# Optimization experiments

Hardware: AMD Instinct MI355X
Metric: run time of the kernel (lower is better)

The kernel has to match this reference:

```python
import jax, jax.numpy as jnp
import numpy as np

N, DIM, RF_DIM, H, W, PN, TOPK = 16, 2048, 256, 16, 8, 64, 10  # TOPK = 2*k = 2*(K//2)


def conv1x1(w, x):
    # w: [O, C] (1x1 conv kernel), x: [b, C, h, w] -> [b, O, h, w]
    return jnp.einsum('oc,bchw->bohw', w, x)


def calibration(x, y):
    # x, y: [b, c, h, w]
    b, c, h, w = x.shape
    xv = x.reshape(b, c, h * w)
    yv = y.reshape(b, c, h * w)
    c_aff = jax.nn.softmax(jnp.einsum('bcm,bdm->bcd', xv, yv), axis=2)  # [b,c,c]
    s_aff = jax.nn.softmax(jnp.einsum('bcm,bcn->bmn', xv, yv), axis=2)  # [b,hw,hw]
    c_avg = c_aff.mean(axis=-1)  # [b,c]
    s_avg = s_aff.mean(axis=-1)  # [b,hw]
    aff = (c_avg[:, :, None] * s_avg[:, None, :]).reshape(b, c, h, w)
    pos = jax.nn.relu(aff - 0.5) + 0.5
    comp = jax.nn.relu(0.5 - aff) + 0.5
    return x * pos + y * comp


def instance_norm(x, eps=1e-5):
    m = x.mean(axis=(2, 3), keepdims=True)
    v = x.var(axis=(2, 3), keepdims=True)
    return (x - m) * jax.lax.rsqrt(v + eps)


def setup_inputs():
    key = jax.random.key(0)
    ks = jax.random.split(key, 6)
    return {
        'inputs': jax.random.normal(ks[0], (N, DIM, H, W), jnp.float32),
        'mv_prototype': jax.random.normal(ks[1], (PN, DIM, H, W), jnp.float32),
        'w_rf': jax.random.normal(ks[2], (RF_DIM, DIM), jnp.float32) * 0.02,
        'w_rf_mv': jax.random.normal(ks[3], (DIM, TOPK * RF_DIM), jnp.float32) * 0.02,
        'w_rm_s': jax.random.normal(ks[4], (DIM, DIM), jnp.float32) * 0.02,
        'w_fuse': jax.random.normal(ks[5], (DIM, DIM), jnp.float32) * 0.02,
    }


def reference(inputs, mv_prototype, w_rf, w_rf_mv, w_rm_s, w_fuse):
    n, c, h, w = inputs.shape
    # pairwise squared euclidean distance (addmm-style cdist)
    xf = inputs.reshape(n, -1)
    pf = mv_prototype.reshape(mv_prototype.shape[0], -1)
    dist = (xf * xf).sum(1, keepdims=True) + (pf * pf).sum(1)[None, :] - 2.0 * xf @ pf.T
    idx = jnp.argsort(dist, axis=1)[:, :TOPK]  # [n, 2k] nearest prototypes
    # refine prototypes then gather per-sample top-2k and stack channels
    xp = conv1x1(w_rf, mv_prototype)  # [pn, rf_dim, h, w]
    mv_list = xp[idx].reshape(n, TOPK * RF_DIM, h, w)
    mvl = conv1x1(w_rf_mv, mv_list)  # [n, dim, h, w]
    mvl = jax.nn.relu(calibration(inputs, mvl))
    mv_a = instance_norm(conv1x1(w_rm_s, mvl))
    x_fuse = jax.nn.sigmoid(conv1x1(w_fuse, mv_a))
    return inputs + inputs * x_fuse
```

## Files before the change

kernel.cpp:

```cpp
#include <hip/hip_runtime.h>
#include <cstdint>
#include <cstddef>

#define N_    16
#define DIM_  2048
#define RF_   256
#define PN_   64
#define TOPK_ 10
#define HW_   128
#define KFULL (DIM_*HW_)
#define KMV   (TOPK_*RF_)

#define AS1 __attribute__((address_space(1)))
#define AS3 __attribute__((address_space(3)))

typedef __attribute__((ext_vector_type(8))) short bf16x8;
typedef __attribute__((ext_vector_type(4))) float f32x4;
typedef __attribute__((ext_vector_type(8))) unsigned short u16x8;

__device__ __forceinline__ unsigned short f2bf(float f) {
  unsigned u = __builtin_bit_cast(unsigned, f);
  unsigned r = (u + 0x7FFFu + ((u >> 16) & 1u)) >> 16;
  return (unsigned short)r;
}

__global__ __launch_bounds__(256)
void front_kernel(const float* __restrict__ x, const float* __restrict__ proto,
                  float* __restrict__ part,
                  unsigned short* __restrict__ protoT, float* __restrict__ pnorm_part,
                  const float* __restrict__ s0, const float* __restrict__ s1,
                  const float* __restrict__ s2, const float* __restrict__ s3,
                  unsigned short* __restrict__ d0, unsigned short* __restrict__ d1,
                  unsigned short* __restrict__ d2, unsigned short* __restrict__ d3,
                  float* __restrict__ dsum) {
  __shared__ alignas(16) unsigned char ldsbuf[43520];
  const int t = threadIdx.x;
  const int bid = blockIdx.x;
  {
    int g = bid * 256 + t;
    if (g < 1152) dsum[g] = 0.f;
  }

  if (bid < 512) {
    float (*xl)[16][68] = (float (*)[16][68])ldsbuf;
    float (*pl)[64][68] = (float (*)[64][68])(ldsbuf + 8704);
    const int b = bid;
    const int n0 = t & 7, pb = t >> 3;
    const int xr = t >> 4, xc = (t & 15) * 4;
    float acc[2][2] = {};
    const size_t kbase = (size_t)b * 512;

    float4 rx, rp[4];
    auto gload = [&](int ph) {
      const size_t k0 = kbase + ph * 64;
      rx = *(const float4*)(x + (size_t)xr * KFULL + k0 + xc);
#pragma unroll
      for (int i = 0; i < 4; ++i) {
        int idx = i * 256 + t;
        rp[i] = *(const float4*)(proto + (size_t)(idx >> 4) * KFULL + k0 + (idx & 15) * 4);
      }
    };
    auto swrite = [&](int buf) {
      *(float4*)&xl[buf][xr][xc] = rx;
#pragma unroll
      for (int i = 0; i < 4; ++i) {
        int idx = i * 256 + t;
        *(float4*)&pl[buf][idx >> 4][(idx & 15) * 4] = rp[i];
      }
    };

    gload(0); swrite(0);
    __syncthreads();
    for (int ph = 0; ph < 8; ++ph) {
      const int buf = ph & 1;
      if (ph + 1 < 8) gload(ph + 1);
#pragma unroll 8
      for (int k = 0; k < 64; k += 4) {
        float4 xa = *(float4*)&xl[buf][n0][k];
        float4 xb = *(float4*)&xl[buf][n0 + 8][k];
        float4 p0 = *(float4*)&pl[buf][pb][k];
        float4 p1 = *(float4*)&pl[buf][pb + 32][k];
        acc[0][0] += xa.x*p0.x + xa.y*p0.y + xa.z*p0.z + xa.w*p0.w;
        acc[0][1] += xa.x*p1.x + xa.y*p1.y + xa.z*p1.z + xa.w*p1.w;
        acc[1][0] += xb.x*p0.x + xb.y*p0.y + xb.z*p0.z + xb.w*p0.w;
        acc[1][1] += xb.x*p1.x + xb.y*p1.y + xb.z*p1.z + xb.w*p1.w;
      }
      if (ph + 1 < 8) swrite(buf ^ 1);
      __syncthreads();
    }

    float* scratch = (float*)ldsbuf;
    scratch[n0 * 64 + pb]            = -2.f * acc[0][0];
    scratch[n0 * 64 + pb + 32]       = -2.f * acc[0][1];
    scratch[(n0 + 8) * 64 + pb]      = -2.f * acc[1][0];
    scratch[(n0 + 8) * 64 + pb + 32] = -2.f * acc[1][1];
    __syncthreads();
    *(float4*)(part + (size_t)b * 1024 + t * 4) = *(const float4*)&scratch[t * 4];

  } else if (bid < 4608) {
    float (*tile)[129] = (float (*)[129])ldsbuf;
    float* ssq = (float*)(ldsbuf + 16512);
    const int local = bid - 512;
    const int p = local & 63;
    const int c0 = (local >> 6) * 32;
    const float* sp = proto + ((size_t)p * DIM_ + c0) * HW_;
    float sq = 0.f;
#pragma unroll
    for (int i = 0; i < 4; ++i) {
      int g = i * 256 + t;
      int ci = g >> 5, s4 = g & 31;
      float4 v = *(const float4*)(sp + (size_t)ci * HW_ + s4 * 4);
      sq += v.x * v.x + v.y * v.y + v.z * v.z + v.w * v.w;
      int sb = s4 * 4;
      tile[ci][sb] = v.x; tile[ci][sb + 1] = v.y; tile[ci][sb + 2] = v.z; tile[ci][sb + 3] = v.w;
    }
#pragma unroll
    for (int m = 1; m < 64; m <<= 1) sq += __shfl_xor(sq, m, 64);
    if ((t & 63) == 0) ssq[t >> 6] = sq;
    __syncthreads();
    if (t == 0) pnorm_part[(local >> 6) * PN_ + p] = ssq[0] + ssq[1] + ssq[2] + ssq[3];
    unsigned short* dp = protoT + (size_t)p * HW_ * DIM_ + (size_t)(c0 >> 3) * 1024;
#pragma unroll
    for (int i = 0; i < 2; ++i) {
      int cidx = i * 256 + t;
      int kg = cidx >> 7, s = cidx & 127;
      u16x8 pk;
#pragma unroll
      for (int u = 0; u < 8; ++u) pk[u] = f2bf(tile[kg * 8 + u][s]);
      *(u16x8*)(dp + (size_t)kg * 1024 + (size_t)s * 8) = pk;
    }

  } else {
    u16x8 (*ctile)[65] = (u16x8 (*)[65])ldsbuf;
    int local = bid - 4608;
    const float* s; unsigned short* d; int O, CG, tb;
    if (local < 32)       { s = s0; d = d0; O = RF_;  CG = DIM_ / 8; tb = local; }
    else if (local < 352) { s = s1; d = d1; O = DIM_; CG = KMV  / 8; tb = local - 32; }
    else if (local < 608) { s = s2; d = d2; O = DIM_; CG = DIM_ / 8; tb = local - 352; }
    else                  { s = s3; d = d3; O = DIM_; CG = DIM_ / 8; tb = local - 608; }
    const int nCgT = CG / 32;
    const int o0  = (tb / nCgT) * 64;
    const int cg0 = (tb % nCgT) * 32;
    const size_t C = (size_t)CG * 8;

#pragma unroll
    for (int i = 0; i < 8; ++i) {
      int idx = i * 256 + t, ol = idx >> 5, cg = idx & 31;
      const float* sp = s + (size_t)(o0 + ol) * C + (size_t)(cg0 + cg) * 8;
      float4 a = *(const float4*)sp;
      float4 b = *(const float4*)(sp + 4);
      u16x8 pk;
      pk[0] = f2bf(a.x); pk[1] = f2bf(a.y); pk[2] = f2bf(a.z); pk[3] = f2bf(a.w);
      pk[4] = f2bf(b.x); pk[5] = f2bf(b.y); pk[6] = f2bf(b.z); pk[7] = f2bf(b.w);
      ctile[cg][ol] = pk;
    }
    __syncthreads();
#pragma unroll
    for (int i = 0; i < 8; ++i) {
      int idx = i * 256 + t, cg = idx >> 6, ol = idx & 63;
      *(u16x8*)(d + (size_t)(cg0 + cg) * ((size_t)O * 8) + (size_t)(o0 + ol) * 8) =
          ctile[cg][ol];
    }
  }
}

__global__ __launch_bounds__(512)
void select_kernel(const float* __restrict__ part, const float* __restrict__ pnorm_part,
                   int* __restrict__ idx, int* __restrict__ flags) {
  __shared__ float red[8][64];
  __shared__ float sh[64];
  const int n = blockIdx.x, t = threadIdx.x;
  const int c = t & 63, ch = t >> 6;
  const float* pp = part + (size_t)ch * 64 * 1024 + n * 64 + c;
  float a0 = 0.f, a1 = 0.f, a2 = 0.f, a3 = 0.f;
  for (int b = 0; b < 64; b += 4) {
    a0 += pp[(size_t)(b + 0) * 1024];
    a1 += pp[(size_t)(b + 1) * 1024];
    a2 += pp[(size_t)(b + 2) * 1024];
    a3 += pp[(size_t)(b + 3) * 1024];
  }
  red[ch][c] = (a0 + a1) + (a2 + a3);
  __syncthreads();
  if (t < 64) {
    float pn = 0.f;
#pragma unroll 8
    for (int cb = 0; cb < DIM_ / 32; ++cb) pn += pnorm_part[cb * PN_ + t];
    float dv = pn;
#pragma unroll
    for (int i = 0; i < 8; ++i) dv += red[i][t];
    sh[t] = dv;
  }
  __syncthreads();
  if (t < 64) {
    float dval = sh[t];
    int rank = 0;
#pragma unroll
    for (int j = 0; j < 64; ++j) {
      float o = sh[j];
      rank += (o < dval || (o == dval && j < t)) ? 1 : 0;
    }
    if (rank < TOPK_) { idx[n * TOPK_ + rank] = t; flags[t] = 1; }
  }
}

#define BM 64
#define BKK 64

template <int MODE>
__global__ __launch_bounds__(512, 4)
void mfma_gemm_kernel(const unsigned short* __restrict__ Wb,
                      const unsigned short* __restrict__ Xb,
                      void* __restrict__ OutP,
                      const float* __restrict__ inputs,
                      const int* __restrict__ idxp,
                      const int* __restrict__ flags,
                      int K, int O, int Ldim) {
  __shared__ alignas(16) unsigned short Al[3][8 * BM * 8];
  __shared__ alignas(16) unsigned short Bl[3][8 * 128 * 8];

  const int t = threadIdx.x;
  const int w = t >> 6;
  const int lane = t & 63;
  const int q = lane >> 4;
  const int l15 = lane & 15;
  const int mq = w >> 1;
  const int h  = w & 1;
  const int batch = blockIdx.y;
  const int o0 = blockIdx.x * BM;

  if (MODE == 0 && flags && !flags[batch]) return;

  int idreg = 0;
  if (MODE == 1 && lane < TOPK_) idreg = idxp[batch * TOPK_ + lane];

  f32x4 acc[4] = {};

  auto issue = [&](int k0, int buf) {
    {
      const unsigned short* ga =
          Wb + (size_t)((k0 >> 3) + w) * (O * 8) + (size_t)(o0 + lane) * 8;
      __builtin_amdgcn_global_load_lds((const AS1 void*)ga,
                                       (AS3 void*)(&Al[buf][w * 512]), 16, 0, 0);
    }
    const unsigned short* base;
    if (MODE == 1) {
      int id = __shfl(idreg, k0 >> 8, 64);
      base = Xb + (size_t)id * (HW_ * RF_) + (size_t)((k0 & 255) >> 3) * 1024;
    } else {
      base = Xb + (size_t)batch * HW_ * K + (size_t)(k0 >> 3) * 1024;
    }
#pragma unroll
    for (int i = 0; i < 2; ++i) {
      int v = w * 2 + i;
      int qk = v >> 1, hh = v & 1;
      const unsigned short* gb = base + (size_t)qk * 1024 + (size_t)(hh * 64 + lane) * 8;
      __builtin_amdgcn_global_load_lds((const AS1 void*)gb,
                                       (AS3 void*)(&Bl[buf][qk * 1024 + hh * 512]), 16, 0, 0);
    }
  };

  const int nIter = K / BKK;

  issue(0, 0);
  issue(BKK, 1);

  for (int it = 0; it < nIter; ++it) {
    const int buf = it % 3;
    if (it + 1 < nIter) {
      asm volatile("s_waitcnt vmcnt(3)" ::: "memory");
    } else {
      asm volatile("s_waitcnt vmcnt(0)" ::: "memory");
    }
    __builtin_amdgcn_s_barrier();
#pragma unroll
    for (int s = 0; s < 2; ++s) {
      bf16x8 af, bfr[4];
      af = *(const bf16x8*)(&Al[buf][(s * 4 + q) * 512 + (mq * 16 + l15) * 8]);
#pragma unroll
      for (int nt = 0; nt < 4; ++nt)
        bfr[nt] = *(const bf16x8*)(&Bl[buf][(s * 4 + q) * 1024 + (h * 64 + nt * 16 + l15) * 8]);
#pragma unroll
      for (int nt = 0; nt < 4; ++nt)
        acc[nt] = __builtin_amdgcn_mfma_f32_16x16x32_bf16(af, bfr[nt], acc[nt], 0, 0, 0);
    }
    if (it + 2 < nIter) issue((it + 2) * BKK, (it + 2) % 3);
  }

  const float CAL = 1.0f - 1.0f / 262144.0f;

  float* nsumS = (float*)&Al[0][0];
  float* nsqS  = (float*)&Al[0][0] + 128;

  if (MODE == 2) {
#pragma unroll
    for (int reg = 0; reg < 4; ++reg) {
      float s_ = 0.f, q_ = 0.f;
#pragma unroll
      for (int nt = 0; nt < 4; ++nt) {
        float v = acc[nt][reg];
        s_ += v; q_ += v * v;
      }
#pragma unroll
      for (int m = 1; m < 16; m <<= 1) {
        s_ += __shfl_xor(s_, m, 64);
        q_ += __shfl_xor(q_, m, 64);
      }
      if (l15 == 0) {
        nsumS[w * 16 + q * 4 + reg] = s_;
        nsqS [w * 16 + q * 4 + reg] = q_;
      }
    }
    __syncthreads();
  }

  if (MODE == 3) {
    float* ofb = (float*)OutP + (size_t)batch * DIM_ * HW_;
    const float* inb = inputs + (size_t)batch * DIM_ * HW_;
#pragma unroll
    for (int nt = 0; nt < 4; ++nt) {
      int o = o0 + mq * 16 + q * 4;
      int s = h * 64 + nt * 16 + l15;
      f32x4 v = acc[nt];
#pragma unroll
      for (int g = 0; g < 4; ++g) {
        float in = inb[(size_t)(o + g) * HW_ + s];
        float sg = 1.f / (1.f + expf(-v[g]));
        ofb[(size_t)(o + g) * HW_ + s] = in * (1.f + sg);
      }
    }
  } else {
    unsigned short* ob = (unsigned short*)OutP + (size_t)batch * HW_ * Ldim;
    const float* inb = (MODE == 1) ? inputs + (size_t)batch * DIM_ * HW_ : nullptr;
    float mean[4], rs[4];
    if (MODE == 2) {
#pragma unroll
      for (int reg = 0; reg < 4; ++reg) {
        int ol = q * 4 + reg;
        float ts = nsumS[(mq * 2 + 0) * 16 + ol] + nsumS[(mq * 2 + 1) * 16 + ol];
        float tq = nsqS [(mq * 2 + 0) * 16 + ol] + nsqS [(mq * 2 + 1) * 16 + ol];
        float mn = ts * (1.f / 128.f);
        float vr = tq * (1.f / 128.f) - mn * mn;
        mean[reg] = mn; rs[reg] = rsqrtf(vr + 1e-5f);
      }
    }
#pragma unroll
    for (int nt = 0; nt < 4; ++nt) {
      int o = o0 + mq * 16 + q * 4;
      int s = h * 64 + nt * 16 + l15;
      f32x4 v = acc[nt];
      float r[4];
      if (MODE == 0) {
#pragma unroll
        for (int g = 0; g < 4; ++g) r[g] = v[g];
      } else if (MODE == 1) {
        const float* ip = inb + (size_t)o * HW_ + s;
#pragma unroll
        for (int g = 0; g < 4; ++g)
          r[g] = fmaxf(0.f, 0.5f * ip[(size_t)g * HW_] + CAL * v[g]);
      } else {
#pragma unroll
        for (int g = 0; g < 4; ++g) r[g] = (v[g] - mean[g]) * rs[g];
      }
      ushort4 pk;
      pk.x = f2bf(r[0]); pk.y = f2bf(r[1]); pk.z = f2bf(r[2]); pk.w = f2bf(r[3]);
      *(ushort4*)(ob + (size_t)(o >> 3) * 1024 + (size_t)s * 8 + (o & 7)) = pk;
    }
  }
}

extern "C" void kernel_launch(void* const* d_in, const int* in_sizes, int n_in,
                              void* d_out, int out_size, void* d_ws, size_t ws_size,
                              hipStream_t stream) {
  const float* inputs = (const float*)d_in[0];
  const float* proto  = (const float*)d_in[1];
  const float* w_rf   = (const float*)d_in[2];
  const float* w_rfmv = (const float*)d_in[3];
  const float* w_rms  = (const float*)d_in[4];
  const float* w_fuse = (const float*)d_in[5];
  float* out = (float*)d_out;

  uint8_t* ws = (uint8_t*)d_ws;
  size_t off = 0;
  auto alloc = [&](size_t bytes) { uint8_t* p = ws + off; off += (bytes + 255) & ~(size_t)255; return p; };

  float* dsum  = (float*)alloc(1088 * 4);
  int*   flags = (int*)alloc(PN_ * 4);
  int*   idx   = (int*)alloc(N_ * TOPK_ * 4);
  float* pnorm = (float*)alloc((size_t)(DIM_ / 32) * PN_ * 4);
  float* part  = (float*)alloc((size_t)512 * 1024 * 4);
  unsigned short* wrf_b   = (unsigned short*)alloc((size_t)RF_ * DIM_ * 2);
  unsigned short* wrfmv_b = (unsigned short*)alloc((size_t)DIM_ * KMV * 2);
  unsigned short* wrms_b  = (unsigned short*)alloc((size_t)DIM_ * DIM_ * 2);
  unsigned short* wfuse_b = (unsigned short*)alloc((size_t)DIM_ * DIM_ * 2);
  unsigned short* xpT     = (unsigned short*)alloc((size_t)PN_ * HW_ * RF_ * 2);
  unsigned short* protoT  = (unsigned short*)alloc((size_t)PN_ * HW_ * DIM_ * 2);
  unsigned short* mvlT = protoT;
  unsigned short* mvaT = protoT + (size_t)N_ * HW_ * DIM_;

  front_kernel<<<5472, 256, 0, stream>>>(inputs, proto, part, protoT, pnorm,
                                         w_rf, w_rfmv, w_rms, w_fuse,
                                         wrf_b, wrfmv_b, wrms_b, wfuse_b, dsum);
  select_kernel<<<N_, 512, 0, stream>>>(part, pnorm, idx, flags);

  mfma_gemm_kernel<0><<<dim3(RF_ / BM, PN_), 512, 0, stream>>>(
      wrf_b, protoT, xpT, nullptr, nullptr, flags, DIM_, RF_, RF_);
  mfma_gemm_kernel<1><<<dim3(DIM_ / BM, N_), 512, 0, stream>>>(
      wrfmv_b, xpT, mvlT, inputs, idx, nullptr, KMV, DIM_, DIM_);
  mfma_gemm_kernel<2><<<dim3(DIM_ / BM, N_), 512, 0, stream>>>(
      wrms_b, mvlT, mvaT, nullptr, nullptr, nullptr, DIM_, DIM_, DIM_);
  mfma_gemm_kernel<3><<<dim3(DIM_ / BM, N_), 512, 0, stream>>>(
      wfuse_b, mvaT, out, inputs, nullptr, nullptr, DIM_, DIM_, DIM_);
}
```

Before: 303.0 us.

## Fuse cdist dot-product into prototype transpose blocks, removing separate distance blocks

The 512 dedicated cross-product blocks are removed. Each prototype transpose block now keeps its loaded prototype slice in registers and dots it against all 16 inputs for the same channel range, writing a much smaller per-channel-block partial array. This lets the prototype be read once instead of twice and shrinks the partial buffer the select kernel reduces. In exchange, each transpose block rereads the input slices, 16 per block and 4096 blocks in total, relying on cache reuse, and does more register and shuffle work per block. Launch bounds with an occupancy hint and a smaller LDS buffer are also set.

```diff
diff --git a/kernel.cpp b/kernel.cpp
--- a/kernel.cpp
+++ b/kernel.cpp
@@ -24,16 +24,16 @@
   return (unsigned short)r;
 }
 
-__global__ __launch_bounds__(256)
+__global__ __launch_bounds__(256, 4)
 void front_kernel(const float* __restrict__ x, const float* __restrict__ proto,
-                  float* __restrict__ part,
                   unsigned short* __restrict__ protoT, float* __restrict__ pnorm_part,
+                  float* __restrict__ part2,
                   const float* __restrict__ s0, const float* __restrict__ s1,
                   const float* __restrict__ s2, const float* __restrict__ s3,
                   unsigned short* __restrict__ d0, unsigned short* __restrict__ d1,
                   unsigned short* __restrict__ d2, unsigned short* __restrict__ d3,
                   float* __restrict__ dsum) {
-  __shared__ alignas(16) unsigned char ldsbuf[43520];
+  __shared__ alignas(16) unsigned char ldsbuf[33280];
   const int t = threadIdx.x;
   const int bid = blockIdx.x;
   {
@@ -41,84 +41,48 @@
     if (g < 1152) dsum[g] = 0.f;
   }
 
-  if (bid < 512) {
-    float (*xl)[16][68] = (float (*)[16][68])ldsbuf;
-    float (*pl)[64][68] = (float (*)[64][68])(ldsbuf + 8704);
-    const int b = bid;
-    const int n0 = t & 7, pb = t >> 3;
-    const int xr = t >> 4, xc = (t & 15) * 4;
-    float acc[2][2] = {};
-    const size_t kbase = (size_t)b * 512;
-
-    float4 rx, rp[4];
-    auto gload = [&](int ph) {
-      const size_t k0 = kbase + ph * 64;
-      rx = *(const float4*)(x + (size_t)xr * KFULL + k0 + xc);
-#pragma unroll
-      for (int i = 0; i < 4; ++i) {
-        int idx = i * 256 + t;
-        rp[i] = *(const float4*)(proto + (size_t)(idx >> 4) * KFULL + k0 + (idx & 15) * 4);
-      }
-    };
-    auto swrite = [&](int buf) {
-      *(float4*)&xl[buf][xr][xc] = rx;
-#pragma unroll
-      for (int i = 0; i < 4; ++i) {
-        int idx = i * 256 + t;
-        *(float4*)&pl[buf][idx >> 4][(idx & 15) * 4] = rp[i];
-      }
-    };
-
-    gload(0); swrite(0);
-    __syncthreads();
-    for (int ph = 0; ph < 8; ++ph) {
-      const int buf = ph & 1;
-      if (ph + 1 < 8) gload(ph + 1);
-#pragma unroll 8
-      for (int k = 0; k < 64; k += 4) {
-        float4 xa = *(float4*)&xl[buf][n0][k];
-        float4 xb = *(float4*)&xl[buf][n0 + 8][k];
-        float4 p0 = *(float4*)&pl[buf][pb][k];
-        float4 p1 = *(float4*)&pl[buf][pb + 32][k];
-        acc[0][0] += xa.x*p0.x + xa.y*p0.y + xa.z*p0.z + xa.w*p0.w;
-        acc[0][1] += xa.x*p1.x + xa.y*p1.y + xa.z*p1.z + xa.w*p1.w;
-        acc[1][0] += xb.x*p0.x + xb.y*p0.y + xb.z*p0.z + xb.w*p0.w;
-        acc[1][1] += xb.x*p1.x + xb.y*p1.y + xb.z*p1.z + xb.w*p1.w;
-      }
-      if (ph + 1 < 8) swrite(buf ^ 1);
-      __syncthreads();
-    }
-
-    float* scratch = (float*)ldsbuf;
-    scratch[n0 * 64 + pb]            = -2.f * acc[0][0];
-    scratch[n0 * 64 + pb + 32]       = -2.f * acc[0][1];
-    scratch[(n0 + 8) * 64 + pb]      = -2.f * acc[1][0];
-    scratch[(n0 + 8) * 64 + pb + 32] = -2.f * acc[1][1];
-    __syncthreads();
-    *(float4*)(part + (size_t)b * 1024 + t * 4) = *(const float4*)&scratch[t * 4];
-
-  } else if (bid < 4608) {
+  if (bid < 4096) {
     float (*tile)[129] = (float (*)[129])ldsbuf;
     float* ssq = (float*)(ldsbuf + 16512);
-    const int local = bid - 512;
-    const int p = local & 63;
-    const int c0 = (local >> 6) * 32;
+    float (*dred)[16] = (float (*)[16])(ldsbuf + 16528);
+    const int p  = bid & 63;
+    const int cb = bid >> 6;
+    const int c0 = cb * 32;
     const float* sp = proto + ((size_t)p * DIM_ + c0) * HW_;
     float sq = 0.f;
+    float4 pv[4];
 #pragma unroll
     for (int i = 0; i < 4; ++i) {
       int g = i * 256 + t;
       int ci = g >> 5, s4 = g & 31;
       float4 v = *(const float4*)(sp + (size_t)ci * HW_ + s4 * 4);
+      pv[i] = v;
       sq += v.x * v.x + v.y * v.y + v.z * v.z + v.w * v.w;
       int sb = s4 * 4;
       tile[ci][sb] = v.x; tile[ci][sb + 1] = v.y; tile[ci][sb + 2] = v.z; tile[ci][sb + 3] = v.w;
     }
+
+    float accn[16];
+#pragma unroll
+    for (int n = 0; n < 16; ++n) accn[n] = 0.f;
+#pragma unroll
+    for (int n = 0; n < 16; ++n) {
+      const float* xb = x + (size_t)n * KFULL + (size_t)c0 * HW_;
+#pragma unroll
+      for (int i = 0; i < 4; ++i) {
+        int g = i * 256 + t;
+        int ci = g >> 5, s4 = g & 31;
+        float4 xv = *(const float4*)(xb + (size_t)ci * HW_ + s4 * 4);
+        accn[n] += xv.x * pv[i].x + xv.y * pv[i].y + xv.z * pv[i].z + xv.w * pv[i].w;
+      }
+    }
+
 #pragma unroll
     for (int m = 1; m < 64; m <<= 1) sq += __shfl_xor(sq, m, 64);
     if ((t & 63) == 0) ssq[t >> 6] = sq;
     __syncthreads();
-    if (t == 0) pnorm_part[(local >> 6) * PN_ + p] = ssq[0] + ssq[1] + ssq[2] + ssq[3];
+    if (t == 0) pnorm_part[cb * PN_ + p] = ssq[0] + ssq[1] + ssq[2] + ssq[3];
+
     unsigned short* dp = protoT + (size_t)p * HW_ * DIM_ + (size_t)(c0 >> 3) * 1024;
 #pragma unroll
     for (int i = 0; i < 2; ++i) {
@@ -130,9 +94,22 @@
       *(u16x8*)(dp + (size_t)kg * 1024 + (size_t)s * 8) = pk;
     }
 
+#pragma unroll
+    for (int n = 0; n < 16; ++n) {
+      float v = accn[n];
+#pragma unroll
+      for (int m = 1; m < 64; m <<= 1) v += __shfl_xor(v, m, 64);
+      if ((t & 63) == 0) dred[t >> 6][n] = v;
+    }
+    __syncthreads();
+    if (t < 16) {
+      float s_ = dred[0][t] + dred[1][t] + dred[2][t] + dred[3][t];
+      part2[((size_t)cb * 64 + p) * 16 + t] = -2.f * s_;
+    }
+
   } else {
     u16x8 (*ctile)[65] = (u16x8 (*)[65])ldsbuf;
-    int local = bid - 4608;
+    int local = bid - 4096;
     const float* s; unsigned short* d; int O, CG, tb;
     if (local < 32)       { s = s0; d = d0; O = RF_;  CG = DIM_ / 8; tb = local; }
     else if (local < 352) { s = s1; d = d1; O = DIM_; CG = KMV  / 8; tb = local - 32; }
@@ -165,21 +142,19 @@
 }
 
 __global__ __launch_bounds__(512)
-void select_kernel(const float* __restrict__ part, const float* __restrict__ pnorm_part,
+void select_kernel(const float* __restrict__ part2, const float* __restrict__ pnorm_part,
                    int* __restrict__ idx, int* __restrict__ flags) {
   __shared__ float red[8][64];
   __shared__ float sh[64];
   const int n = blockIdx.x, t = threadIdx.x;
   const int c = t & 63, ch = t >> 6;
-  const float* pp = part + (size_t)ch * 64 * 1024 + n * 64 + c;
-  float a0 = 0.f, a1 = 0.f, a2 = 0.f, a3 = 0.f;
-  for (int b = 0; b < 64; b += 4) {
-    a0 += pp[(size_t)(b + 0) * 1024];
-    a1 += pp[(size_t)(b + 1) * 1024];
-    a2 += pp[(size_t)(b + 2) * 1024];
-    a3 += pp[(size_t)(b + 3) * 1024];
-  }
-  red[ch][c] = (a0 + a1) + (a2 + a3);
+  float a = 0.f;
+#pragma unroll
+  for (int j = 0; j < 8; ++j) {
+    int cb = ch + j * 8;
+    a += part2[((size_t)cb * 64 + c) * 16 + n];
+  }
+  red[ch][c] = a;
   __syncthreads();
   if (t < 64) {
     float pn = 0.f;
@@ -387,7 +362,7 @@
   int*   flags = (int*)alloc(PN_ * 4);
   int*   idx   = (int*)alloc(N_ * TOPK_ * 4);
   float* pnorm = (float*)alloc((size_t)(DIM_ / 32) * PN_ * 4);
-  float* part  = (float*)alloc((size_t)512 * 1024 * 4);
+  float* part2 = (float*)alloc((size_t)64 * 64 * 16 * 4);
   unsigned short* wrf_b   = (unsigned short*)alloc((size_t)RF_ * DIM_ * 2);
   unsigned short* wrfmv_b = (unsigned short*)alloc((size_t)DIM_ * KMV * 2);
   unsigned short* wrms_b  = (unsigned short*)alloc((size_t)DIM_ * DIM_ * 2);
@@ -397,10 +372,10 @@
   unsigned short* mvlT = protoT;
   unsigned short* mvaT = protoT + (size_t)N_ * HW_ * DIM_;
 
-  front_kernel<<<5472, 256, 0, stream>>>(inputs, proto, part, protoT, pnorm,
+  front_kernel<<<4960, 256, 0, stream>>>(inputs, proto, protoT, pnorm, part2,
                                          w_rf, w_rfmv, w_rms, w_fuse,
                                          wrf_b, wrfmv_b, wrms_b, wfuse_b, dsum);
-  select_kernel<<<N_, 512, 0, stream>>>(part, pnorm, idx, flags);
+  select_kernel<<<N_, 512, 0, stream>>>(part2, pnorm, idx, flags);
 
   mfma_gemm_kernel<0><<<dim3(RF_ / BM, PN_), 512, 0, stream>>>(
       wrf_b, protoT, xpT, nullptr, nullptr, flags, DIM_, RF_, RF_);
```

Measured after the change: 754.2 us. 149% more time.
